# Kernel tuning notes

Hardware: AMD Instinct MI355X
Metric: run time of the kernel (lower is better)

## Reference

```python
import jax, jax.numpy as jnp
import numpy as np

BS = 8
ALPHA = 0.1
BETA = 0.05


def setup_inputs() -> dict:
    key = jax.random.key(0)
    H, W = 8192, 8192
    frame = jax.random.uniform(key, (H, W), dtype=jnp.float32)
    return {"frame": frame}


def _vertical_pass(frame, bs, alpha, beta):
    # Boundary columns x in range(bs, W-1, bs). bs>=2 so x>=2 and x<W-1 always.
    W = frame.shape[1]
    cols = jnp.arange(bs, W - 1, bs)
    p1 = frame[:, cols - 2]  # (H, nb)
    p0 = frame[:, cols - 1]
    q0 = frame[:, cols]
    q1 = frame[:, cols + 1]
    mask = (jnp.abs(p0 - q0) < alpha) & (jnp.abs(p1 - p0) < beta) & (jnp.abs(q1 - q0) < beta)
    p0_new = (2 * p1 + p0 + q0 + 2) / 4
    q0_new = (2 * q1 + q0 + p0 + 2) / 4
    out = frame.at[:, cols - 1].set(jnp.where(mask, p0_new, p0))
    out = out.at[:, cols].set(jnp.where(mask, q0_new, q0))
    return out


def _horizontal_pass(frame, bs, alpha, beta):
    H = frame.shape[0]
    rows = jnp.arange(bs, H - 1, bs)
    p1 = frame[rows - 2, :]  # (nb, W)
    p0 = frame[rows - 1, :]
    q0 = frame[rows, :]
    q1 = frame[rows + 1, :]
    mask = (jnp.abs(p0 - q0) < alpha) & (jnp.abs(p1 - p0) < beta) & (jnp.abs(q1 - q0) < beta)
    p0_new = (2 * p1 + p0 + q0 + 2) / 4
    q0_new = (2 * q1 + q0 + p0 + 2) / 4
    out = frame.at[rows - 1, :].set(jnp.where(mask, p0_new, p0))
    out = out.at[rows, :].set(jnp.where(mask, q0_new, q0))
    return out


def reference(frame):
    # Pass 1 reads the original frame, writes vertical-boundary updates.
    stage1 = _vertical_pass(frame, BS, ALPHA, BETA)
    # Pass 2 reads the stage-1 result (frame = output.clone() in the original).
    out = _horizontal_pass(stage1, BS, ALPHA, BETA)
    return out
```

## Files before the change

### kernel.cpp

```cpp
#include <hip/hip_runtime.h>
#include <math.h>


static constexpr int W = 8192;
static constexpr int H = 8192;
#define ALPHA 0.1f
#define BETA  0.05f

__device__ __forceinline__ bool dmask(float p1, float p0, float q0, float q1) {
    return (fabsf(p0 - q0) < ALPHA) && (fabsf(p1 - p0) < BETA) && (fabsf(q1 - q0) < BETA);
}

__device__ __forceinline__ float filt_p(float p1, float p0, float q0, float q1) {
    float v = (((2.0f * p1 + p0) + q0) + 2.0f) * 0.25f;
    return dmask(p1, p0, q0, q1) ? v : p0;
}
__device__ __forceinline__ float filt_q(float p1, float p0, float q0, float q1) {
    float v = (((2.0f * q1 + q0) + p0) + 2.0f) * 0.25f;
    return dmask(p1, p0, q0, q1) ? v : q0;
}

struct Vec8 { float v[8]; };

__device__ __forceinline__ Vec8 stage1_row8(const float* __restrict__ row, int j0) {
    const float4 a = *reinterpret_cast<const float4*>(row + j0);
    const float4 b = *reinterpret_cast<const float4*>(row + j0 + 4);
    Vec8 r;
    r.v[0] = a.x; r.v[1] = a.y; r.v[2] = a.z; r.v[3] = a.w;
    r.v[4] = b.x; r.v[5] = b.y; r.v[6] = b.z; r.v[7] = b.w;
    if (j0 != 0) {
        const float2 pm = *reinterpret_cast<const float2*>(row + j0 - 2);
        r.v[0] = filt_q(pm.x, pm.y, a.x, a.y);
    }
    if (j0 + 8 != W) {
        const float2 qn = *reinterpret_cast<const float2*>(row + j0 + 8);
        r.v[7] = filt_p(b.z, b.w, qn.x, qn.y);
    }
    return r;
}

__global__ __launch_bounds__(256)
void deblock_fused(const float* __restrict__ in, float* __restrict__ out) {
    const int j0 = (blockIdx.x * blockDim.x + threadIdx.x) * 8;
    const int i  = blockIdx.y;
    const float* row = in + (size_t)i * W;
    const int m8 = i & 7;
    Vec8 r;
    if (m8 == 7 && i != H - 1) {
        Vec8 s0 = stage1_row8(row - W, j0);
        Vec8 s1 = stage1_row8(row, j0);
        Vec8 s2 = stage1_row8(row + W, j0);
        Vec8 s3 = stage1_row8(row + 2 * (size_t)W, j0);
        #pragma unroll
        for (int k = 0; k < 8; ++k) r.v[k] = filt_p(s0.v[k], s1.v[k], s2.v[k], s3.v[k]);
    } else if (m8 == 0 && i != 0) {
        Vec8 s0 = stage1_row8(row - 2 * (size_t)W, j0);
        Vec8 s1 = stage1_row8(row - W, j0);
        Vec8 s2 = stage1_row8(row, j0);
        Vec8 s3 = stage1_row8(row + W, j0);
        #pragma unroll
        for (int k = 0; k < 8; ++k) r.v[k] = filt_q(s0.v[k], s1.v[k], s2.v[k], s3.v[k]);
    } else {
        r = stage1_row8(row, j0);
    }
    float* orow = out + (size_t)i * W + j0;
    *reinterpret_cast<float4*>(orow)     = make_float4(r.v[0], r.v[1], r.v[2], r.v[3]);
    *reinterpret_cast<float4*>(orow + 4) = make_float4(r.v[4], r.v[5], r.v[6], r.v[7]);
}

extern "C" void kernel_launch(void* const* d_in, const int* in_sizes, int n_in,
                              void* d_out, int out_size, void* d_ws, size_t ws_size,
                              hipStream_t stream) {
    const float* frame = (const float*)d_in[0];
    float* out = (float*)d_out;
    dim3 block(256, 1, 1);
    dim3 grid(W / (256 * 8), H, 1);
    deblock_fused<<<grid, block, 0, stream>>>(frame, out);
}
```

Measured before the change: 521.6 us.

## Process one 8-row band per thread to reuse vertical-pass rows across boundaries

Each thread now handles a strip of rows, from row 8k+1 through row 8k+8, instead of a single row. The stage-1 (vertical) results for the four rows around each horizontal boundary are computed once and shared between the p-side and q-side outputs. The old code had boundary rows recompute four stage-1 rows each. This cuts redundant loads and ALU work and gives each thread more work. In exchange the grid has 8x fewer blocks and each thread issues more sequential row accesses, which lowers parallelism.

```diff
diff --git a/kernel.cpp b/kernel.cpp
--- a/kernel.cpp
+++ b/kernel.cpp
@@ -10,7 +10,6 @@
 __device__ __forceinline__ bool dmask(float p1, float p0, float q0, float q1) {
     return (fabsf(p0 - q0) < ALPHA) && (fabsf(p1 - p0) < BETA) && (fabsf(q1 - q0) < BETA);
 }
-
 __device__ __forceinline__ float filt_p(float p1, float p0, float q0, float q1) {
     float v = (((2.0f * p1 + p0) + q0) + 2.0f) * 0.25f;
     return dmask(p1, p0, q0, q1) ? v : p0;
@@ -39,33 +38,43 @@
     return r;
 }
 
+__device__ __forceinline__ void store8(float* __restrict__ p, const Vec8& s) {
+    *reinterpret_cast<float4*>(p)     = make_float4(s.v[0], s.v[1], s.v[2], s.v[3]);
+    *reinterpret_cast<float4*>(p + 4) = make_float4(s.v[4], s.v[5], s.v[6], s.v[7]);
+}
+
 __global__ __launch_bounds__(256)
-void deblock_fused(const float* __restrict__ in, float* __restrict__ out) {
+void deblock_tiled(const float* __restrict__ in, float* __restrict__ out) {
     const int j0 = (blockIdx.x * blockDim.x + threadIdx.x) * 8;
-    const int i  = blockIdx.y;
-    const float* row = in + (size_t)i * W;
-    const int m8 = i & 7;
-    Vec8 r;
-    if (m8 == 7 && i != H - 1) {
-        Vec8 s0 = stage1_row8(row - W, j0);
-        Vec8 s1 = stage1_row8(row, j0);
-        Vec8 s2 = stage1_row8(row + W, j0);
-        Vec8 s3 = stage1_row8(row + 2 * (size_t)W, j0);
+    const int k  = blockIdx.y;
+    const size_t base = (size_t)(8 * k) * W;
+
+    Vec8 s6;
+    #pragma unroll
+    for (int r = 1; r <= 6; ++r) {
+        Vec8 s = stage1_row8(in + base + (size_t)r * W, j0);
+        if (r == 6) s6 = s;
+        store8(out + base + (size_t)r * W + j0, s);
+    }
+
+    if (k != H / 8 - 1) {
+        Vec8 s7 = stage1_row8(in + base + (size_t)7 * W, j0);
+        Vec8 s8 = stage1_row8(in + base + (size_t)8 * W, j0);
+        Vec8 s9 = stage1_row8(in + base + (size_t)9 * W, j0);
+        Vec8 rp, rq;
         #pragma unroll
-        for (int k = 0; k < 8; ++k) r.v[k] = filt_p(s0.v[k], s1.v[k], s2.v[k], s3.v[k]);
-    } else if (m8 == 0 && i != 0) {
-        Vec8 s0 = stage1_row8(row - 2 * (size_t)W, j0);
-        Vec8 s1 = stage1_row8(row - W, j0);
-        Vec8 s2 = stage1_row8(row, j0);
-        Vec8 s3 = stage1_row8(row + W, j0);
-        #pragma unroll
-        for (int k = 0; k < 8; ++k) r.v[k] = filt_q(s0.v[k], s1.v[k], s2.v[k], s3.v[k]);
+        for (int c = 0; c < 8; ++c) {
+            rp.v[c] = filt_p(s6.v[c], s7.v[c], s8.v[c], s9.v[c]);
+            rq.v[c] = filt_q(s6.v[c], s7.v[c], s8.v[c], s9.v[c]);
+        }
+        store8(out + base + (size_t)7 * W + j0, rp);
+        store8(out + base + (size_t)8 * W + j0, rq);
     } else {
-        r = stage1_row8(row, j0);
+        Vec8 s7 = stage1_row8(in + base + (size_t)7 * W, j0);
+        store8(out + base + (size_t)7 * W + j0, s7);
+        Vec8 s0 = stage1_row8(in, j0);
+        store8(out + j0, s0);
     }
-    float* orow = out + (size_t)i * W + j0;
-    *reinterpret_cast<float4*>(orow)     = make_float4(r.v[0], r.v[1], r.v[2], r.v[3]);
-    *reinterpret_cast<float4*>(orow + 4) = make_float4(r.v[4], r.v[5], r.v[6], r.v[7]);
 }
 
 extern "C" void kernel_launch(void* const* d_in, const int* in_sizes, int n_in,
@@ -74,6 +83,6 @@
     const float* frame = (const float*)d_in[0];
     float* out = (float*)d_out;
     dim3 block(256, 1, 1);
-    dim3 grid(W / (256 * 8), H, 1);
-    deblock_fused<<<grid, block, 0, stream>>>(frame, out);
+    dim3 grid(W / 8 / 256, H / 8, 1);
+    deblock_tiled<<<grid, block, 0, stream>>>(frame, out);
 }
```

After: 466.8 us. -10.5%, faster.
